# Kernel tuning notes

Measured on AMD Instinct MI355X. Metric: run time of the kernel, lower is better.

## Reference

```python
import jax, jax.numpy as jnp
import numpy as np

N_GRIDS, N_FEATS = 64, 2
GD = GH = GW = 64
PE_TERMS, N_DIMS = 6, 3
NODES, N_OUT = 64, 1
N_PTS = 524288


def setup_inputs() -> dict:
    key = jax.random.key(0)
    ks = jax.random.split(key, 8)
    x = jax.random.uniform(ks[0], (N_PTS, N_DIMS), jnp.float32, -1.0, 1.0)
    grid_scales = jax.random.uniform(ks[1], (N_GRIDS, 3), jnp.float32, 1.0, 4.0)
    grid_translations = jax.random.uniform(ks[2], (N_GRIDS, 3), jnp.float32, -1.0, 1.0) * (grid_scales - 1.0)
    feature_grids = jax.random.normal(ks[3], (N_GRIDS, N_FEATS, GD, GH, GW), jnp.float32)
    d_in = PE_TERMS * N_DIMS * 2 + N_FEATS * N_GRIDS  # 36 + 128 = 164
    W0 = jax.random.normal(ks[4], (d_in, NODES), jnp.float32) * np.sqrt(2.0 / (d_in + NODES))
    b0 = jnp.zeros((NODES,), jnp.float32)
    W1 = jax.random.normal(ks[5], (NODES, NODES), jnp.float32) * np.sqrt(2.0 / (2 * NODES))
    b1 = jnp.zeros((NODES,), jnp.float32)
    W2 = jax.random.normal(ks[6], (NODES, N_OUT), jnp.float32) * np.sqrt(2.0 / (NODES + N_OUT))
    b2 = jnp.zeros((N_OUT,), jnp.float32)
    return dict(x=x, grid_scales=grid_scales, grid_translations=grid_translations,
                feature_grids=feature_grids, W0=W0, b0=b0, W1=W1, b1=b1, W2=W2, b2=b2)


def grid_sample_3d(vol, coords):
    """Trilinear grid_sample, align_corners=True, padding_mode='zeros'.
    vol: [C,D,H,W]; coords: [N,3] in (x,y,z) order (x -> W axis), range [-1,1].
    Returns [C,N]."""
    C, D, H, W = vol.shape
    flat = vol.reshape(C, D * H * W)
    ix = (coords[:, 0] + 1.0) * 0.5 * (W - 1)
    iy = (coords[:, 1] + 1.0) * 0.5 * (H - 1)
    iz = (coords[:, 2] + 1.0) * 0.5 * (D - 1)
    x0 = jnp.floor(ix); y0 = jnp.floor(iy); z0 = jnp.floor(iz)
    wx = ix - x0; wy = iy - y0; wz = iz - z0
    x0i = x0.astype(jnp.int32); y0i = y0.astype(jnp.int32); z0i = z0.astype(jnp.int32)
    out = jnp.zeros((C, coords.shape[0]), vol.dtype)
    for dz, wz_ in ((0, 1.0 - wz), (1, wz)):
        for dy, wy_ in ((0, 1.0 - wy), (1, wy)):
            for dx, wx_ in ((0, 1.0 - wx), (1, wx)):
                xi = x0i + dx; yi = y0i + dy; zi = z0i + dz
                valid = (xi >= 0) & (xi < W) & (yi >= 0) & (yi < H) & (zi >= 0) & (zi < D)
                idx = (jnp.clip(zi, 0, D - 1) * H + jnp.clip(yi, 0, H - 1)) * W + jnp.clip(xi, 0, W - 1)
                v = jnp.take(flat, idx, axis=1) * valid.astype(vol.dtype)[None, :]
                out = out + v * (wz_ * wy_ * wx_)[None, :]
    return out


def positional_encoding(x):
    # NeRF-style PE: sin/cos of pi*2^i * x, i in [0, PE_TERMS), out dim = 2*L*3
    freqs = jnp.pi * (2.0 ** jnp.arange(PE_TERMS, dtype=jnp.float32))  # [L]
    ang = x[:, None, :] * freqs[None, :, None]                          # [N,L,3]
    n = x.shape[0]
    return jnp.concatenate([jnp.sin(ang).reshape(n, -1), jnp.cos(ang).reshape(n, -1)], axis=1)


def snake_alt(x):
    return 0.5 * x + jnp.sin(x) ** 2


def reference(x, grid_scales, grid_translations, feature_grids, W0, b0, W1, b1, W2, b2):
    # per-grid affine transform (equivalent to bmm with the scale+translation 4x4)
    tp = x[None, :, :] * grid_scales[:, None, :] + grid_translations[:, None, :]  # [G,N,3]
    feats = jax.vmap(grid_sample_3d)(feature_grids, tp)  # [G,C,N]
    G, C, N = feats.shape
    feats = feats.reshape(G * C, N).T                    # [N, G*C]
    pe = positional_encoding(x)                          # [N, 2*L*3]
    y = jnp.concatenate([pe, feats], axis=1)
    y = snake_alt(y @ W0 + b0)
    y = snake_alt(y @ W1 + b1)
    y = y @ W2 + b2
    return y
```

## Files before the change

kernel.cpp:

```cpp
#include <hip/hip_runtime.h>
#include <hip/hip_bf16.h>

#define NPTS    524288
#define NG      64
#define GSZ     64
#define VOX     (GSZ*GSZ*GSZ)
#define NODES   64
#define TILE    64
#define NBLK    (NPTS / TILE)
#define K0      192
#define SF      200
#define NCELL   4096
#define PREP_VB 16384
#define PREP_CB 2048

typedef __attribute__((ext_vector_type(8))) short bf16x8;
typedef __attribute__((ext_vector_type(4))) float f32x4;

__device__ inline unsigned short f2bf(float f) {
    __hip_bfloat16 b = __float2bfloat16(f);
    union { __hip_bfloat16 h; unsigned short u; } cv; cv.h = b;
    return cv.u;
}
__device__ inline unsigned int pk2(float c0, float c1) {
    return (unsigned int)f2bf(c0) | ((unsigned int)f2bf(c1) << 16);
}
__device__ inline float bflo(unsigned int v) { return __uint_as_float(v << 16); }
__device__ inline float bfhi(unsigned int v) { return __uint_as_float(v & 0xffff0000u); }

__device__ inline int spread4(int v) {
    return (v & 1) | ((v & 2) << 2) | ((v & 4) << 4) | ((v & 8) << 6);
}
__device__ inline int cell_of(float px, float py, float pz) {
    int cx = min(max((int)((px + 1.0f) * 8.0f), 0), 15);
    int cy = min(max((int)((py + 1.0f) * 8.0f), 0), 15);
    int cz = min(max((int)((pz + 1.0f) * 8.0f), 0), 15);
    return spread4(cx) | (spread4(cy) << 1) | (spread4(cz) << 2);
}


__global__ void prep_fused(const float* __restrict__ fg, uint4* __restrict__ vox4,
                           const float* __restrict__ x, unsigned short* __restrict__ cid,
                           int* __restrict__ hist,
                           const float* __restrict__ W0, const float* __restrict__ W1,
                           unsigned short* __restrict__ w0t, unsigned short* __restrict__ w1t) {
    int b = blockIdx.x;
    int tid = threadIdx.x;
    if (b < PREP_VB) {
        int idx = b * 256 + tid;
        int g = idx >> 16;
        int hb = idx & 65535;
        int brick = hb >> 1;
        int h = hb & 1;
        int bx = brick & 31, by = (brick >> 5) & 31, bz = brick >> 10;
        int xx = bx << 1, yy = by << 1, zz = (bz << 1) + h;
        const float* c0 = fg + (size_t)g * (2 * VOX) + ((zz << 6) + yy) * 64 + xx;
        const float* c1 = c0 + VOX;
        float2 a0 = *(const float2*)c0;
        float2 a1 = *(const float2*)(c0 + 64);
        float2 d0 = *(const float2*)c1;
        float2 d1 = *(const float2*)(c1 + 64);
        vox4[idx] = make_uint4(pk2(a0.x, d0.x), pk2(a0.y, d0.y),
                               pk2(a1.x, d1.x), pk2(a1.y, d1.y));
    } else if (b < PREP_VB + PREP_CB) {
        int p = (b - PREP_VB) * 256 + tid;
        int c = cell_of(x[p * 3 + 0], x[p * 3 + 1], x[p * 3 + 2]);
        cid[p] = (unsigned short)c;
        atomicAdd(&hist[c], 1);
    } else {
        int t = (b - PREP_VB - PREP_CB) * 256 + tid;
        for (int i = t; i < NODES * K0; i += 4096) {
            int n = i / K0, k = i - n * K0;
            w0t[i] = (k < 164) ? f2bf(W0[k * NODES + n]) : (unsigned short)0;
        }
        for (int i = t; i < NODES * NODES; i += 4096) {
            int n = i >> 6, k = i & 63;
            w1t[i] = f2bf(W1[k * NODES + n]);
        }
    }
}

__global__ void sort_scan(const int* __restrict__ hist, int* __restrict__ offs) {
    __shared__ int partial[256];
    int t = threadIdx.x;
    int loc[16];
    int s = 0;
    #pragma unroll
    for (int i = 0; i < 16; ++i) { loc[i] = s; s += hist[t * 16 + i]; }
    partial[t] = s;
    __syncthreads();
    for (int d = 1; d < 256; d <<= 1) {
        int v = (t >= d) ? partial[t - d] : 0;
        __syncthreads();
        partial[t] += v;
        __syncthreads();
    }
    int base = partial[t] - s;
    #pragma unroll
    for (int i = 0; i < 16; ++i) offs[t * 16 + i] = base + loc[i];
}

__global__ void sort_scatter(const float* __restrict__ x, const unsigned short* __restrict__ cell_id,
                             int* __restrict__ offs, float4* __restrict__ spts) {
    int p = blockIdx.x * blockDim.x + threadIdx.x;
    int c = cell_id[p];
    int pos = atomicAdd(&offs[c], 1);
    spts[pos] = make_float4(x[p * 3 + 0], x[p * 3 + 1], x[p * 3 + 2], __int_as_float(p));
}

struct GP {
    int xp0, xp1, yp0, yp1, zp0, zp1;
    float wx0, wx1, wy0, wy1, wz0, wz1;
    const unsigned int* vg;
};
__device__ inline GP gprep(int g, float ix, float iy, float iz,
                           const unsigned int* __restrict__ vox) {
    GP p;
    float fx = floorf(ix), fy = floorf(iy), fz = floorf(iz);
    int x0 = (int)fx, y0 = (int)fy, z0 = (int)fz;
    float wx = ix - fx, wy = iy - fy, wz = iz - fz;
    p.wx0 = (x0 >= 0) ? (1.0f - wx) : 0.0f;
    p.wx1 = (x0 < 63) ? wx : 0.0f;
    p.wy0 = (y0 >= 0) ? (1.0f - wy) : 0.0f;
    p.wy1 = (y0 < 63) ? wy : 0.0f;
    p.wz0 = (z0 >= 0) ? (1.0f - wz) : 0.0f;
    p.wz1 = (z0 < 63) ? wz : 0.0f;
    int xc0 = max(x0, 0), xc1 = min(x0 + 1, 63);
    int yc0 = max(y0, 0), yc1 = min(y0 + 1, 63);
    int zc0 = max(z0, 0), zc1 = min(z0 + 1, 63);
    p.xp0 = ((xc0 >> 1) << 3) | (xc0 & 1);
    p.xp1 = ((xc1 >> 1) << 3) | (xc1 & 1);
    p.yp0 = ((yc0 >> 1) << 8) | ((yc0 & 1) << 1);
    p.yp1 = ((yc1 >> 1) << 8) | ((yc1 & 1) << 1);
    p.zp0 = ((zc0 >> 1) << 13) | ((zc0 & 1) << 2);
    p.zp1 = ((zc1 >> 1) << 13) | ((zc1 & 1) << 2);
    p.vg = vox + ((size_t)g << 18);
    return p;
}

__device__ inline void gather2(int pt, int gA, float axi, float ayi, float azi, bool wrA,
                               int gB, float bxi, float byi, float bzi, bool wrB,
                               const unsigned int* __restrict__ vox,
                               unsigned short* Fsh) {
    GP a = gprep(gA, axi, ayi, azi, vox);
    GP b = gprep(gB, bxi, byi, bzi, vox);
    unsigned int a00 = a.vg[a.zp0 + a.yp0 + a.xp0], a01 = a.vg[a.zp0 + a.yp0 + a.xp1];
    unsigned int a10 = a.vg[a.zp0 + a.yp1 + a.xp0], a11 = a.vg[a.zp0 + a.yp1 + a.xp1];
    unsigned int a20 = a.vg[a.zp1 + a.yp0 + a.xp0], a21 = a.vg[a.zp1 + a.yp0 + a.xp1];
    unsigned int a30 = a.vg[a.zp1 + a.yp1 + a.xp0], a31 = a.vg[a.zp1 + a.yp1 + a.xp1];
    unsigned int b00 = b.vg[b.zp0 + b.yp0 + b.xp0], b01 = b.vg[b.zp0 + b.yp0 + b.xp1];
    unsigned int b10 = b.vg[b.zp0 + b.yp1 + b.xp0], b11 = b.vg[b.zp0 + b.yp1 + b.xp1];
    unsigned int b20 = b.vg[b.zp1 + b.yp0 + b.xp0], b21 = b.vg[b.zp1 + b.yp0 + b.xp1];
    unsigned int b30 = b.vg[b.zp1 + b.yp1 + b.xp0], b31 = b.vg[b.zp1 + b.yp1 + b.xp1];
    {
        float f0 = 0.f, f1 = 0.f, wzy;
        wzy = a.wz0 * a.wy0;
        f0 += wzy * (a.wx0 * bflo(a00) + a.wx1 * bflo(a01));
        f1 += wzy * (a.wx0 * bfhi(a00) + a.wx1 * bfhi(a01));
        wzy = a.wz0 * a.wy1;
        f0 += wzy * (a.wx0 * bflo(a10) + a.wx1 * bflo(a11));
        f1 += wzy * (a.wx0 * bfhi(a10) + a.wx1 * bfhi(a11));
        wzy = a.wz1 * a.wy0;
        f0 += wzy * (a.wx0 * bflo(a20) + a.wx1 * bflo(a21));
        f1 += wzy * (a.wx0 * bfhi(a20) + a.wx1 * bfhi(a21));
        wzy = a.wz1 * a.wy1;
        f0 += wzy * (a.wx0 * bflo(a30) + a.wx1 * bflo(a31));
        f1 += wzy * (a.wx0 * bfhi(a30) + a.wx1 * bfhi(a31));
        if (wrA) *(unsigned int*)&Fsh[pt * SF + 36 + 2 * gA] = pk2(f0, f1);
    }
    {
        float f0 = 0.f, f1 = 0.f, wzy;
        wzy = b.wz0 * b.wy0;
        f0 += wzy * (b.wx0 * bflo(b00) + b.wx1 * bflo(b01));
        f1 += wzy * (b.wx0 * bfhi(b00) + b.wx1 * bfhi(b01));
        wzy = b.wz0 * b.wy1;
        f0 += wzy * (b.wx0 * bflo(b10) + b.wx1 * bflo(b11));
        f1 += wzy * (b.wx0 * bfhi(b10) + b.wx1 * bfhi(b11));
        wzy = b.wz1 * b.wy0;
        f0 += wzy * (b.wx0 * bflo(b20) + b.wx1 * bflo(b21));
        f1 += wzy * (b.wx0 * bfhi(b20) + b.wx1 * bfhi(b21));
        wzy = b.wz1 * b.wy1;
        f0 += wzy * (b.wx0 * bflo(b30) + b.wx1 * bflo(b31));
        f1 += wzy * (b.wx0 * bfhi(b30) + b.wx1 * bfhi(b31));
        if (wrB) *(unsigned int*)&Fsh[pt * SF + 36 + 2 * gB] = pk2(f0, f1);
    }
}

__device__ inline void gather1(int pt, int g, float ix, float iy, float iz, bool wr,
                               const unsigned int* __restrict__ vox,
                               unsigned short* Fsh) {
    GP a = gprep(g, ix, iy, iz, vox);
    unsigned int a00 = a.vg[a.zp0 + a.yp0 + a.xp0], a01 = a.vg[a.zp0 + a.yp0 + a.xp1];
    unsigned int a10 = a.vg[a.zp0 + a.yp1 + a.xp0], a11 = a.vg[a.zp0 + a.yp1 + a.xp1];
    unsigned int a20 = a.vg[a.zp1 + a.yp0 + a.xp0], a21 = a.vg[a.zp1 + a.yp0 + a.xp1];
    unsigned int a30 = a.vg[a.zp1 + a.yp1 + a.xp0], a31 = a.vg[a.zp1 + a.yp1 + a.xp1];
    float f0 = 0.f, f1 = 0.f, wzy;
    wzy = a.wz0 * a.wy0;
    f0 += wzy * (a.wx0 * bflo(a00) + a.wx1 * bflo(a01));
    f1 += wzy * (a.wx0 * bfhi(a00) + a.wx1 * bfhi(a01));
    wzy = a.wz0 * a.wy1;
    f0 += wzy * (a.wx0 * bflo(a10) + a.wx1 * bflo(a11));
    f1 += wzy * (a.wx0 * bfhi(a10) + a.wx1 * bfhi(a11));
    wzy = a.wz1 * a.wy0;
    f0 += wzy * (a.wx0 * bflo(a20) + a.wx1 * bflo(a21));
    f1 += wzy * (a.wx0 * bfhi(a20) + a.wx1 * bfhi(a21));
    wzy = a.wz1 * a.wy1;
    f0 += wzy * (a.wx0 * bflo(a30) + a.wx1 * bflo(a31));
    f1 += wzy * (a.wx0 * bfhi(a30) + a.wx1 * bfhi(a31));
    if (wr) *(unsigned int*)&Fsh[pt * SF + 36 + 2 * g] = pk2(f0, f1);
}

__global__ void __launch_bounds__(256, 5)
amrsrn_main(const float4* __restrict__ spts,
            const float* __restrict__ gscale,
            const float* __restrict__ gtrans,
            const unsigned int* __restrict__ vox,
            const unsigned short* __restrict__ w0t,
            const unsigned short* __restrict__ w1t,
            const float* __restrict__ b0,
            const float* __restrict__ b1,
            const float* __restrict__ W2,
            const float* __restrict__ b2,
            float* __restrict__ out) {
    __shared__ unsigned short Fsh[TILE * SF];
    __shared__ int   sidx[TILE];
    __shared__ float gss[NG * 3];
    __shared__ float gts[NG * 3];

    const int tid = threadIdx.x;
    const int lane = tid & 63;
    const int wv = tid >> 6;
    const int cb = ((blockIdx.x >> 8) << 8) | ((blockIdx.x & 7) << 5) | ((blockIdx.x >> 3) & 31);
    const int base = cb * TILE;

    for (int i = tid; i < TILE * SF / 8; i += 256) ((uint4*)Fsh)[i] = make_uint4(0,0,0,0);
    float4 sp = spts[base + lane];
    const float px = sp.x, py = sp.y, pz = sp.z;
    if (tid < TILE) sidx[tid] = __float_as_int(sp.w);
    if (tid < NG * 3) { gss[tid] = gscale[tid]; gts[tid] = gtrans[tid]; }
    __syncthreads();

    float lox = px, hix = px, loy = py, hiy = py, loz = pz, hiz = pz;
    #pragma unroll
    for (int m = 1; m < 64; m <<= 1) {
        lox = fminf(lox, __shfl_xor(lox, m)); hix = fmaxf(hix, __shfl_xor(hix, m));
        loy = fminf(loy, __shfl_xor(loy, m)); hiy = fmaxf(hiy, __shfl_xor(hiy, m));
        loz = fminf(loz, __shfl_xor(loz, m)); hiz = fmaxf(hiz, __shfl_xor(hiz, m));
    }
    unsigned long long mfull, mpart;
    {
        int g = lane;
        float s0 = gss[g*3+0], s1 = gss[g*3+1], s2 = gss[g*3+2];
        float t0 = gts[g*3+0], t1 = gts[g*3+1], t2 = gts[g*3+2];
        float xl = (lox*s0 + t0 + 1.0f)*31.5f, xh = (hix*s0 + t0 + 1.0f)*31.5f;
        float yl = (loy*s1 + t1 + 1.0f)*31.5f, yh = (hiy*s1 + t1 + 1.0f)*31.5f;
        float zl = (loz*s2 + t2 + 1.0f)*31.5f, zh = (hiz*s2 + t2 + 1.0f)*31.5f;
        bool fullg = (xl >= -0.999f) & (xh <= 63.999f)
                   & (yl >= -0.999f) & (yh <= 63.999f)
                   & (zl >= -0.999f) & (zh <= 63.999f);
        bool outg  = (xh < -1.001f) | (xl >= 64.001f)
                   | (yh < -1.001f) | (yl >= 64.001f)
                   | (zh < -1.001f) | (zl >= 64.001f);
        mfull = __ballot(fullg);
        mpart = __ballot(!fullg && !outg);
    }

    {
        #pragma unroll
        for (int t = 0; t < 9; ++t) {
            int tau = wv * 9 + t;
            int tt = (tau < 18) ? tau : tau - 18;
            int l = tt / 3, d = tt - l * 3;
            float c = (d == 0) ? px : ((d == 1) ? py : pz);
            float ang = c * (3.14159265358979323846f * (float)(1 << l));
            float val = (tau < 18) ? __sinf(ang) : __cosf(ang);
            Fsh[lane * SF + tau] = f2bf(val);
        }
    }

    {
        int idx = 0;
        int gq = -1; float qx = 0.f, qy = 0.f, qz = 0.f; bool qw = false;
        #pragma unroll 1
        for (int pass = 0; pass < 2; ++pass) {
            unsigned long long m = pass ? mpart : mfull;
            while (m) {
                int g = __builtin_ctzll(m);
                m &= m - 1;
                if ((idx++ & 3) != wv) continue;
                float ix = (px * gss[g*3+0] + gts[g*3+0] + 1.0f) * 31.5f;
                float iy = (py * gss[g*3+1] + gts[g*3+1] + 1.0f) * 31.5f;
                float iz = (pz * gss[g*3+2] + gts[g*3+2] + 1.0f) * 31.5f;
                bool wr = true;
                if (pass) {
                    wr = (ix >= -1.0f) & (ix < 64.0f)
                       & (iy >= -1.0f) & (iy < 64.0f)
                       & (iz >= -1.0f) & (iz < 64.0f);
                }
                if (gq < 0) { gq = g; qx = ix; qy = iy; qz = iz; qw = wr; }
                else {
                    gather2(lane, gq, qx, qy, qz, qw, g, ix, iy, iz, wr, vox, Fsh);
                    gq = -1;
                }
            }
        }
        if (gq >= 0) gather1(lane, gq, qx, qy, qz, qw, vox, Fsh);
    }
    __syncthreads();

    const int ptb = wv * 16;
    const int row = lane & 15;
    const int quad = lane >> 4;
    const int koff = quad * 8;

    f32x4 acc0[4] = {{0,0,0,0},{0,0,0,0},{0,0,0,0},{0,0,0,0}};
    #pragma unroll
    for (int ks = 0; ks < 6; ++ks) {
        bf16x8 a = *(const bf16x8*)&Fsh[(ptb + row) * SF + ks * 32 + koff];
        #pragma unroll
        for (int nt = 0; nt < 4; ++nt) {
            bf16x8 b = *(const bf16x8*)&w0t[(nt * 16 + row) * K0 + ks * 32 + koff];
            acc0[nt] = __builtin_amdgcn_mfma_f32_16x16x32_bf16(a, b, acc0[nt], 0, 0, 0);
        }
    }
    #pragma unroll
    for (int nt = 0; nt < 4; ++nt) {
        int node = nt * 16 + row;
        float bb = b0[node];
        #pragma unroll
        for (int r = 0; r < 4; ++r) {
            float h = acc0[nt][r] + bb;
            float s = __sinf(h);
            h = 0.5f * h + s * s;
            Fsh[(ptb + quad * 4 + r) * SF + node] = f2bf(h);
        }
    }

    f32x4 acc1[4] = {{0,0,0,0},{0,0,0,0},{0,0,0,0},{0,0,0,0}};
    #pragma unroll
    for (int ks = 0; ks < 2; ++ks) {
        bf16x8 a = *(const bf16x8*)&Fsh[(ptb + row) * SF + ks * 32 + koff];
        #pragma unroll
        for (int nt = 0; nt < 4; ++nt) {
            bf16x8 b = *(const bf16x8*)&w1t[(nt * 16 + row) * NODES + ks * 32 + koff];
            acc1[nt] = __builtin_amdgcn_mfma_f32_16x16x32_bf16(a, b, acc1[nt], 0, 0, 0);
        }
    }
    float part[4] = {0.f, 0.f, 0.f, 0.f};
    #pragma unroll
    for (int nt = 0; nt < 4; ++nt) {
        int node = nt * 16 + row;
        float b1v = b1[node];
        float w2v = W2[node];
        #pragma unroll
        for (int r = 0; r < 4; ++r) {
            float h = acc1[nt][r] + b1v;
            float s = __sinf(h);
            h = 0.5f * h + s * s;
            part[r] += h * w2v;
        }
    }
    #pragma unroll
    for (int m = 1; m < 16; m <<= 1) {
        #pragma unroll
        for (int r = 0; r < 4; ++r) part[r] += __shfl_xor(part[r], m);
    }
    if (row == 0) {
        float b2v = b2[0];
        #pragma unroll
        for (int r = 0; r < 4; ++r) {
            int pt = ptb + quad * 4 + r;
            out[sidx[pt]] = part[r] + b2v;
        }
    }
}

__global__ void amrsrn_fallback(const float* __restrict__ x,
                                const float* __restrict__ gscale,
                                const float* __restrict__ gtrans,
                                const float* __restrict__ fg,
                                const float* __restrict__ W0,
                                const float* __restrict__ b0,
                                const float* __restrict__ W1,
                                const float* __restrict__ b1,
                                const float* __restrict__ W2,
                                const float* __restrict__ b2,
                                float* __restrict__ out) {
    int p = blockIdx.x * blockDim.x + threadIdx.x;
    float px = x[p*3+0], py = x[p*3+1], pz = x[p*3+2];
    float h0[NODES];
    #pragma unroll
    for (int j = 0; j < NODES; ++j) h0[j] = b0[j];
    #pragma unroll
    for (int l = 0; l < 6; ++l) {
        float freq = 3.14159265358979323846f * (float)(1 << l);
        #pragma unroll
        for (int d = 0; d < 3; ++d) {
            float v = (d == 0 ? px : (d == 1 ? py : pz)) * freq;
            float s = __sinf(v), c = __cosf(v);
            const float* wrs = W0 + (l*3 + d) * NODES;
            const float* wrc = W0 + (18 + l*3 + d) * NODES;
            #pragma unroll
            for (int j = 0; j < NODES; ++j) h0[j] += s * wrs[j] + c * wrc[j];
        }
    }
    for (int g = 0; g < NG; ++g) {
        float ix = (px * gscale[g*3+0] + gtrans[g*3+0] + 1.0f) * 31.5f;
        float iy = (py * gscale[g*3+1] + gtrans[g*3+1] + 1.0f) * 31.5f;
        float iz = (pz * gscale[g*3+2] + gtrans[g*3+2] + 1.0f) * 31.5f;
        float fxf = floorf(ix), fyf = floorf(iy), fzf = floorf(iz);
        int x0 = (int)fxf, y0 = (int)fyf, z0 = (int)fzf;
        float wx = ix - fxf, wy = iy - fyf, wz = iz - fzf;
        bool any = (x0 >= -1 && x0 < GSZ) && (y0 >= -1 && y0 < GSZ) && (z0 >= -1 && z0 < GSZ);
        if (any) {
            float f0 = 0.f, f1 = 0.f;
            #pragma unroll
            for (int dz = 0; dz < 2; ++dz) {
                int zi = z0 + dz; bool vz = ((unsigned)zi < (unsigned)GSZ);
                int zc = min(max(zi, 0), GSZ - 1);
                float wzf = dz ? wz : 1.f - wz;
                #pragma unroll
                for (int dy = 0; dy < 2; ++dy) {
                    int yi = y0 + dy; bool vy = ((unsigned)yi < (unsigned)GSZ);
                    int yc = min(max(yi, 0), GSZ - 1);
                    float wyf = dy ? wy : 1.f - wy;
                    int rowoff = (zc * GSZ + yc) * GSZ;
                    #pragma unroll
                    for (int dx = 0; dx < 2; ++dx) {
                        int xi = x0 + dx; bool vx = ((unsigned)xi < (unsigned)GSZ);
                        int xc = min(max(xi, 0), GSZ - 1);
                        float w = wzf * wyf * (dx ? wx : 1.f - wx);
                        w = (vz && vy && vx) ? w : 0.f;
                        const float* gp = fg + ((size_t)g << 19);
                        f0 += w * gp[rowoff + xc];
                        f1 += w * gp[VOX + rowoff + xc];
                    }
                }
            }
            const float* wr = W0 + (36 + 2*g) * NODES;
            #pragma unroll
            for (int j = 0; j < NODES; ++j) h0[j] += f0 * wr[j] + f1 * wr[NODES + j];
        }
    }
    #pragma unroll
    for (int j = 0; j < NODES; ++j) { float s = __sinf(h0[j]); h0[j] = 0.5f * h0[j] + s * s; }
    float out_acc = b2[0];
    #pragma unroll
    for (int half = 0; half < 2; ++half) {
        float h1[32];
        #pragma unroll
        for (int j = 0; j < 32; ++j) h1[j] = b1[half*32 + j];
        #pragma unroll
        for (int i = 0; i < NODES; ++i) {
            float a = h0[i];
            const float* w1r = W1 + i * NODES + half*32;
            #pragma unroll
            for (int j = 0; j < 32; ++j) h1[j] += a * w1r[j];
        }
        #pragma unroll
        for (int j = 0; j < 32; ++j) { float s = __sinf(h1[j]); out_acc += (0.5f * h1[j] + s * s) * W2[half*32 + j]; }
    }
    out[p] = out_acc;
}

extern "C" void kernel_launch(void* const* d_in, const int* in_sizes, int n_in,
                              void* d_out, int out_size, void* d_ws, size_t ws_size,
                              hipStream_t stream) {
    const float* x      = (const float*)d_in[0];
    const float* gscale = (const float*)d_in[1];
    const float* gtrans = (const float*)d_in[2];
    const float* fg     = (const float*)d_in[3];
    const float* W0     = (const float*)d_in[4];
    const float* b0     = (const float*)d_in[5];
    const float* W1     = (const float*)d_in[6];
    const float* b1     = (const float*)d_in[7];
    const float* W2     = (const float*)d_in[8];
    const float* b2     = (const float*)d_in[9];
    float* out = (float*)d_out;

    char* wsp = (char*)d_ws;
    unsigned short* w0t = (unsigned short*)wsp;
    unsigned short* w1t = w0t + NODES * K0;
    int* hist           = (int*)(wsp + (64 << 10));
    int* offs           = (int*)(wsp + (80 << 10));
    unsigned short* cid = (unsigned short*)(wsp + (96 << 10));
    float4* spts        = (float4*)(wsp + (96 << 10) + (1 << 20));
    unsigned int* vox   = (unsigned int*)(wsp + (96 << 10) + (1 << 20) + (8 << 20));
    const size_t ws_needed = (96 << 10) + (1 << 20) + (8 << 20) + (size_t)NG * VOX * 4;

    if (ws_size >= ws_needed) {
        hipMemsetAsync(hist, 0, NCELL * sizeof(int), stream);
        prep_fused<<<PREP_VB + PREP_CB + 16, 256, 0, stream>>>(
            fg, (uint4*)vox, x, cid, hist, W0, W1, w0t, w1t);
        sort_scan<<<1, 256, 0, stream>>>(hist, offs);
        sort_scatter<<<NPTS / 256, 256, 0, stream>>>(x, cid, offs, spts);
        amrsrn_main<<<NBLK, 256, 0, stream>>>(spts, gscale, gtrans, vox,
                                              w0t, w1t, b0, b1, W2, b2, out);
    } else {
        amrsrn_fallback<<<NPTS / 256, 256, 0, stream>>>(
            x, gscale, gtrans, fg, W0, b0, W1, b1, W2, b2, out);
    }
}
```

Baseline: 448.1 us.

## Give each wave its own 16 points, drop block barriers, pre-swizzle MFMA weights

Result: faster. 395.4 us (-11.8%).

```diff
diff --git a/kernel.cpp b/kernel.cpp
--- a/kernel.cpp
+++ b/kernel.cpp
@@ -43,7 +43,7 @@
                            const float* __restrict__ x, unsigned short* __restrict__ cid,
                            int* __restrict__ hist,
                            const float* __restrict__ W0, const float* __restrict__ W1,
-                           unsigned short* __restrict__ w0t, unsigned short* __restrict__ w1t) {
+                           unsigned short* __restrict__ w0f, unsigned short* __restrict__ w1f) {
     int b = blockIdx.x;
     int tid = threadIdx.x;
     if (b < PREP_VB) {
@@ -69,13 +69,18 @@
         atomicAdd(&hist[c], 1);
     } else {
         int t = (b - PREP_VB - PREP_CB) * 256 + tid;
-        for (int i = t; i < NODES * K0; i += 4096) {
-            int n = i / K0, k = i - n * K0;
-            w0t[i] = (k < 164) ? f2bf(W0[k * NODES + n]) : (unsigned short)0;
-        }
-        for (int i = t; i < NODES * NODES; i += 4096) {
-            int n = i >> 6, k = i & 63;
-            w1t[i] = f2bf(W1[k * NODES + n]);
+        for (int i = t; i < 24 * 512; i += 4096) {
+            int j = i & 7, ln = (i >> 3) & 63, fi = i >> 9;
+            int ks = fi >> 2, nt = fi & 3;
+            int k = ks * 32 + ((ln >> 4) << 3) + j, n = nt * 16 + (ln & 15);
+            w0f[i] = (k < 164) ? f2bf(W0[k * NODES + n]) : (unsigned short)0;
+        }
+        {
+            int i = t;
+            int j = i & 7, ln = (i >> 3) & 63, fi = i >> 9;
+            int ks = fi >> 2, nt = fi & 3;
+            int k = ks * 32 + ((ln >> 4) << 3) + j, n = nt * 16 + (ln & 15);
+            w1f[i] = f2bf(W1[k * NODES + n]);
         }
     }
 }
@@ -210,35 +215,54 @@
     if (wr) *(unsigned int*)&Fsh[pt * SF + 36 + 2 * g] = pk2(f0, f1);
 }
 
-__global__ void __launch_bounds__(256, 5)
+#define EXTRACT(gv, pv) \
+    if (mf) { gv = (int)__builtin_ctzll(mf); mf &= mf - 1; pv = false; } \
+    else if (mp) { gv = (int)__builtin_ctzll(mp); mp &= mp - 1; pv = true; } \
+    else { gv = 0; pv = true; }
+
+__global__ void __launch_bounds__(256, 6)
 amrsrn_main(const float4* __restrict__ spts,
             const float* __restrict__ gscale,
             const float* __restrict__ gtrans,
             const unsigned int* __restrict__ vox,
-            const unsigned short* __restrict__ w0t,
-            const unsigned short* __restrict__ w1t,
+            const unsigned short* __restrict__ w0f,
+            const unsigned short* __restrict__ w1f,
             const float* __restrict__ b0,
             const float* __restrict__ b1,
             const float* __restrict__ W2,
             const float* __restrict__ b2,
             float* __restrict__ out) {
     __shared__ unsigned short Fsh[TILE * SF];
-    __shared__ int   sidx[TILE];
-    __shared__ float gss[NG * 3];
-    __shared__ float gts[NG * 3];
 
     const int tid = threadIdx.x;
     const int lane = tid & 63;
     const int wv = tid >> 6;
-    const int cb = ((blockIdx.x >> 8) << 8) | ((blockIdx.x & 7) << 5) | ((blockIdx.x >> 3) & 31);
+    const int cb = ((blockIdx.x & 7) << 10) | (blockIdx.x >> 3);
     const int base = cb * TILE;
-
-    for (int i = tid; i < TILE * SF / 8; i += 256) ((uint4*)Fsh)[i] = make_uint4(0,0,0,0);
-    float4 sp = spts[base + lane];
+    const int ptb = wv * 16;
+    const int ptloc = lane >> 2;
+    const int sub = lane & 3;
+    const int pt = ptb + ptloc;
+
+    float4 sp = spts[base + pt];
     const float px = sp.x, py = sp.y, pz = sp.z;
-    if (tid < TILE) sidx[tid] = __float_as_int(sp.w);
-    if (tid < NG * 3) { gss[tid] = gscale[tid]; gts[tid] = gtrans[tid]; }
-    __syncthreads();
+    const int sreg = __float_as_int(sp.w);
+
+    {
+        uint4* zp = (uint4*)(Fsh + ptb * SF);
+        for (int i = lane; i < 16 * SF / 8; i += 64) zp[i] = make_uint4(0, 0, 0, 0);
+    }
+
+    #pragma unroll
+    for (int t = 0; t < 9; ++t) {
+        int tau = sub * 9 + t;
+        int tt = (tau < 18) ? tau : tau - 18;
+        int l = tt / 3, d = tt - l * 3;
+        float c = (d == 0) ? px : ((d == 1) ? py : pz);
+        float ang = c * (3.14159265358979323846f * (float)(1 << l));
+        float val = (tau < 18) ? __sinf(ang) : __cosf(ang);
+        Fsh[pt * SF + tau] = f2bf(val);
+    }
 
     float lox = px, hix = px, loy = py, hiy = py, loz = pz, hiz = pz;
     #pragma unroll
@@ -247,11 +271,11 @@
         loy = fminf(loy, __shfl_xor(loy, m)); hiy = fmaxf(hiy, __shfl_xor(hiy, m));
         loz = fminf(loz, __shfl_xor(loz, m)); hiz = fmaxf(hiz, __shfl_xor(hiz, m));
     }
-    unsigned long long mfull, mpart;
+    unsigned long long mf, mp;
     {
         int g = lane;
-        float s0 = gss[g*3+0], s1 = gss[g*3+1], s2 = gss[g*3+2];
-        float t0 = gts[g*3+0], t1 = gts[g*3+1], t2 = gts[g*3+2];
+        float s0 = gscale[g*3+0], s1 = gscale[g*3+1], s2 = gscale[g*3+2];
+        float t0 = gtrans[g*3+0], t1 = gtrans[g*3+1], t2 = gtrans[g*3+2];
         float xl = (lox*s0 + t0 + 1.0f)*31.5f, xh = (hix*s0 + t0 + 1.0f)*31.5f;
         float yl = (loy*s1 + t1 + 1.0f)*31.5f, yh = (hiy*s1 + t1 + 1.0f)*31.5f;
         float zl = (loz*s2 + t2 + 1.0f)*31.5f, zh = (hiz*s2 + t2 + 1.0f)*31.5f;
@@ -261,65 +285,54 @@
         bool outg  = (xh < -1.001f) | (xl >= 64.001f)
                    | (yh < -1.001f) | (yl >= 64.001f)
                    | (zh < -1.001f) | (zl >= 64.001f);
-        mfull = __ballot(fullg);
-        mpart = __ballot(!fullg && !outg);
+        mf = __ballot(fullg);
+        mp = __ballot(!fullg && !outg);
     }
 
     {
-        #pragma unroll
-        for (int t = 0; t < 9; ++t) {
-            int tau = wv * 9 + t;
-            int tt = (tau < 18) ? tau : tau - 18;
-            int l = tt / 3, d = tt - l * 3;
-            float c = (d == 0) ? px : ((d == 1) ? py : pz);
-            float ang = c * (3.14159265358979323846f * (float)(1 << l));
-            float val = (tau < 18) ? __sinf(ang) : __cosf(ang);
-            Fsh[lane * SF + tau] = f2bf(val);
-        }
-    }
-
-    {
-        int idx = 0;
-        int gq = -1; float qx = 0.f, qy = 0.f, qz = 0.f; bool qw = false;
-        #pragma unroll 1
-        for (int pass = 0; pass < 2; ++pass) {
-            unsigned long long m = pass ? mpart : mfull;
-            while (m) {
-                int g = __builtin_ctzll(m);
-                m &= m - 1;
-                if ((idx++ & 3) != wv) continue;
-                float ix = (px * gss[g*3+0] + gts[g*3+0] + 1.0f) * 31.5f;
-                float iy = (py * gss[g*3+1] + gts[g*3+1] + 1.0f) * 31.5f;
-                float iz = (pz * gss[g*3+2] + gts[g*3+2] + 1.0f) * 31.5f;
-                bool wr = true;
-                if (pass) {
-                    wr = (ix >= -1.0f) & (ix < 64.0f)
-                       & (iy >= -1.0f) & (iy < 64.0f)
-                       & (iz >= -1.0f) & (iz < 64.0f);
-                }
-                if (gq < 0) { gq = g; qx = ix; qy = iy; qz = iz; qw = wr; }
-                else {
-                    gather2(lane, gq, qx, qy, qz, qw, g, ix, iy, iz, wr, vox, Fsh);
-                    gq = -1;
-                }
+        int total = __popcll(mf) + __popcll(mp);
+        int done = 0;
+        while (done < total) {
+            int g0,g1,g2,g3,g4,g5,g6,g7; bool p0,p1,p2,p3,p4,p5,p6,p7;
+            EXTRACT(g0,p0) EXTRACT(g1,p1) EXTRACT(g2,p2) EXTRACT(g3,p3)
+            EXTRACT(g4,p4) EXTRACT(g5,p5) EXTRACT(g6,p6) EXTRACT(g7,p7)
+            int  gA = sub==0?g0: sub==1?g1: sub==2?g2:g3;
+            bool pA = sub==0?p0: sub==1?p1: sub==2?p2:p3;
+            bool avA = (done + sub) < total;
+            float ixA = (px * gscale[gA*3+0] + gtrans[gA*3+0] + 1.0f) * 31.5f;
+            float iyA = (py * gscale[gA*3+1] + gtrans[gA*3+1] + 1.0f) * 31.5f;
+            float izA = (pz * gscale[gA*3+2] + gtrans[gA*3+2] + 1.0f) * 31.5f;
+            bool wrA = avA && (!pA || ((ixA >= -1.0f) & (ixA < 64.0f)
+                                     & (iyA >= -1.0f) & (iyA < 64.0f)
+                                     & (izA >= -1.0f) & (izA < 64.0f)));
+            if (done + 4 < total) {
+                int  gB = sub==0?g4: sub==1?g5: sub==2?g6:g7;
+                bool pB = sub==0?p4: sub==1?p5: sub==2?p6:p7;
+                bool avB = (done + 4 + sub) < total;
+                float ixB = (px * gscale[gB*3+0] + gtrans[gB*3+0] + 1.0f) * 31.5f;
+                float iyB = (py * gscale[gB*3+1] + gtrans[gB*3+1] + 1.0f) * 31.5f;
+                float izB = (pz * gscale[gB*3+2] + gtrans[gB*3+2] + 1.0f) * 31.5f;
+                bool wrB = avB && (!pB || ((ixB >= -1.0f) & (ixB < 64.0f)
+                                         & (iyB >= -1.0f) & (iyB < 64.0f)
+                                         & (izB >= -1.0f) & (izB < 64.0f)));
+                gather2(pt, gA, ixA, iyA, izA, wrA, gB, ixB, iyB, izB, wrB, vox, Fsh);
+            } else {
+                gather1(pt, gA, ixA, iyA, izA, wrA, vox, Fsh);
             }
-        }
-        if (gq >= 0) gather1(lane, gq, qx, qy, qz, qw, vox, Fsh);
-    }
-    __syncthreads();
-
-    const int ptb = wv * 16;
+            done += 8;
+        }
+    }
+
     const int row = lane & 15;
     const int quad = lane >> 4;
-    const int koff = quad * 8;
 
     f32x4 acc0[4] = {{0,0,0,0},{0,0,0,0},{0,0,0,0},{0,0,0,0}};
     #pragma unroll
     for (int ks = 0; ks < 6; ++ks) {
-        bf16x8 a = *(const bf16x8*)&Fsh[(ptb + row) * SF + ks * 32 + koff];
+        bf16x8 a = *(const bf16x8*)&Fsh[(ptb + row) * SF + ks * 32 + quad * 8];
         #pragma unroll
         for (int nt = 0; nt < 4; ++nt) {
-            bf16x8 b = *(const bf16x8*)&w0t[(nt * 16 + row) * K0 + ks * 32 + koff];
+            bf16x8 b = *(const bf16x8*)&w0f[(((ks << 2) + nt) << 9) + (lane << 3)];
             acc0[nt] = __builtin_amdgcn_mfma_f32_16x16x32_bf16(a, b, acc0[nt], 0, 0, 0);
         }
     }
@@ -339,10 +352,10 @@
     f32x4 acc1[4] = {{0,0,0,0},{0,0,0,0},{0,0,0,0},{0,0,0,0}};
     #pragma unroll
     for (int ks = 0; ks < 2; ++ks) {
-        bf16x8 a = *(const bf16x8*)&Fsh[(ptb + row) * SF + ks * 32 + koff];
+        bf16x8 a = *(const bf16x8*)&Fsh[(ptb + row) * SF + ks * 32 + quad * 8];
         #pragma unroll
         for (int nt = 0; nt < 4; ++nt) {
-            bf16x8 b = *(const bf16x8*)&w1t[(nt * 16 + row) * NODES + ks * 32 + koff];
+            bf16x8 b = *(const bf16x8*)&w1f[(((ks << 2) + nt) << 9) + (lane << 3)];
             acc1[nt] = __builtin_amdgcn_mfma_f32_16x16x32_bf16(a, b, acc1[nt], 0, 0, 0);
         }
     }
@@ -365,13 +378,16 @@
         #pragma unroll
         for (int r = 0; r < 4; ++r) part[r] += __shfl_xor(part[r], m);
     }
+    int o0 = __shfl(sreg, (quad * 4 + 0) << 2);
+    int o1 = __shfl(sreg, (quad * 4 + 1) << 2);
+    int o2 = __shfl(sreg, (quad * 4 + 2) << 2);
+    int o3 = __shfl(sreg, (quad * 4 + 3) << 2);
     if (row == 0) {
         float b2v = b2[0];
-        #pragma unroll
-        for (int r = 0; r < 4; ++r) {
-            int pt = ptb + quad * 4 + r;
-            out[sidx[pt]] = part[r] + b2v;
-        }
+        out[o0] = part[0] + b2v;
+        out[o1] = part[1] + b2v;
+        out[o2] = part[2] + b2v;
+        out[o3] = part[3] + b2v;
     }
 }
 
@@ -479,8 +495,8 @@
     float* out = (float*)d_out;
 
     char* wsp = (char*)d_ws;
-    unsigned short* w0t = (unsigned short*)wsp;
-    unsigned short* w1t = w0t + NODES * K0;
+    unsigned short* w0f = (unsigned short*)wsp;
+    unsigned short* w1f = w0f + 24 * 512;
     int* hist           = (int*)(wsp + (64 << 10));
     int* offs           = (int*)(wsp + (80 << 10));
     unsigned short* cid = (unsigned short*)(wsp + (96 << 10));
@@ -491,11 +507,11 @@
     if (ws_size >= ws_needed) {
         hipMemsetAsync(hist, 0, NCELL * sizeof(int), stream);
         prep_fused<<<PREP_VB + PREP_CB + 16, 256, 0, stream>>>(
-            fg, (uint4*)vox, x, cid, hist, W0, W1, w0t, w1t);
+            fg, (uint4*)vox, x, cid, hist, W0, W1, w0f, w1f);
         sort_scan<<<1, 256, 0, stream>>>(hist, offs);
         sort_scatter<<<NPTS / 256, 256, 0, stream>>>(x, cid, offs, spts);
         amrsrn_main<<<NBLK, 256, 0, stream>>>(spts, gscale, gtrans, vox,
-                                              w0t, w1t, b0, b1, W2, b2, out);
+                                              w0f, w1f, b0, b1, W2, b2, out);
     } else {
         amrsrn_fallback<<<NPTS / 256, 256, 0, stream>>>(
             x, gscale, gtrans, fg, W0, b0, W1, b1, W2, b2, out);
```
